# Kernel tuning notes

Hardware: AMD Instinct MI355X
Metric: run time of the kernel (lower is better)

The kernel has to match this reference:

```python
import jax, jax.numpy as jnp
import numpy as np

D, H, KVH, HD = 2048, 16, 8, 128
D1, D2 = 32, 64  # get_decompose_dim(2048)
BITS = 8


def fake_quant(x, bits=BITS):
    # per-row (last-axis) symmetric fake quant with straight-through estimator
    qmax = float(2 ** (bits - 1) - 1)
    s = jnp.maximum(jnp.max(jnp.abs(x), axis=-1, keepdims=True) / qmax, 1e-8)
    q = jnp.clip(jnp.round(x / s), -qmax, qmax) * s
    return x + jax.lax.stop_gradient(q - x)


def rotate_half(x):
    h = x.shape[-1] // 2
    return jnp.concatenate([-x[..., h:], x[..., :h]], axis=-1)


def setup_inputs() -> dict:
    key = jax.random.key(0)
    ks = jax.random.split(key, 10)
    B, S = 1, 2048
    hidden_states = jax.random.normal(ks[0], (B, S, D), jnp.float32)
    # rotary embeddings
    inv_freq = 1.0 / (10000.0 ** (jnp.arange(0, HD, 2, dtype=jnp.float32) / HD))
    t = jnp.arange(S, dtype=jnp.float32)
    freqs = t[:, None] * inv_freq[None, :]
    emb = jnp.concatenate([freqs, freqs], axis=-1)
    cos, sin = jnp.cos(emb)[None], jnp.sin(emb)[None]  # [1,S,HD]
    # projection weights
    Wq = jax.random.normal(ks[1], (H * HD, D), jnp.float32) * 0.02
    Wk = jax.random.normal(ks[2], (KVH * HD, D), jnp.float32) * 0.02
    Wv = jax.random.normal(ks[3], (KVH * HD, D), jnp.float32) * 0.02
    Wo = jax.random.normal(ks[4], (D, H * HD), jnp.float32) * 0.02
    # learned invertible transforms (near-identity for conditioning)
    L = jnp.eye(D1) + 0.02 * jax.random.normal(ks[5], (D1, D1), jnp.float32)
    R = jnp.eye(D2) + 0.02 * jax.random.normal(ks[6], (D2, D2), jnp.float32)
    diag = 1.0 + 0.1 * jax.random.uniform(ks[7], (D,), jnp.float32)
    Tk = jnp.eye(HD) + 0.02 * jax.random.normal(ks[8], (HD, HD), jnp.float32)
    Tv = jnp.eye(HD) + 0.02 * jax.random.normal(ks[9], (HD, HD), jnp.float32)
    return dict(hidden_states=hidden_states, cos=cos, sin=sin, Wq=Wq, Wk=Wk,
                Wv=Wv, Wo=Wo, L=L, R=R, diag=diag, Tk=Tk, Tv=Tv)


def reference(hidden_states, cos, sin, Wq, Wk, Wv, Wo, L, R, diag, Tk, Tv):
    B, S, _ = hidden_states.shape
    groups = H // KVH
    scale = HD ** -0.5
    # ---- ln_trans: x' = (x * diag) @ kron(L, R) ----
    P = diag[:, None] * jnp.kron(L, R)               # [D, D]
    Pinv = jnp.kron(jnp.linalg.inv(L), jnp.linalg.inv(R)) * (1.0 / diag)[None, :]
    x = hidden_states @ P
    x_q = fake_quant(x)                               # per-token activation quant
    # ---- QKV with transform fused into weights (qa_trans), then weight quant ----
    q = x_q @ fake_quant(Wq @ Pinv.T).T               # [B,S,H*HD]
    k = x_q @ fake_quant(Wk @ Pinv.T).T               # [B,S,KVH*HD]
    Wv_eff = jnp.einsum('hd,khD->kdD', Tv, (Wv @ Pinv.T).reshape(KVH, HD, D))
    v = x_q @ fake_quant(Wv_eff.reshape(KVH * HD, D)).T  # v already in Tv space
    # ---- heads + RoPE ----
    q = q.reshape(B, S, H, HD).transpose(0, 2, 1, 3)
    k = k.reshape(B, S, KVH, HD).transpose(0, 2, 1, 3)
    v = v.reshape(B, S, KVH, HD).transpose(0, 2, 1, 3)
    c, s_ = cos[:, None], sin[:, None]                # [1,1,S,HD]
    q = q * c + rotate_half(q) * s_
    k = k * c + rotate_half(k) * s_
    # ---- kcache trans + quant: q @ inv(Tk)^T, k @ Tk (dot product preserved) ----
    q = q @ jnp.linalg.inv(Tk).T
    k = fake_quant(k @ Tk)
    v = fake_quant(v)
    # ---- eager causal attention with GQA ----
    k = jnp.repeat(k, groups, axis=1)
    v = jnp.repeat(v, groups, axis=1)
    scores = jnp.einsum('bhqd,bhkd->bhqk', q, k) * scale
    mask = jnp.tril(jnp.ones((S, S), bool))
    scores = jnp.where(mask, scores, jnp.finfo(scores.dtype).min)
    w = jax.nn.softmax(scores, axis=-1)
    o = jnp.einsum('bhqk,bhkd->bhqd', w, v)
    o = o.transpose(0, 2, 1, 3).reshape(B, S, H * HD)
    # ---- undo vcache trans per head, then quantized o_proj ----
    o = (o.reshape(B, S, H, HD) @ jnp.linalg.inv(Tv)).reshape(B, S, H * HD)
    out = fake_quant(o) @ fake_quant(Wo).T
    return out
```

## Files before the change

### kernel.cpp

```cpp
#include <hip/hip_runtime.h>
#include <math.h>

typedef unsigned short u16;
typedef __attribute__((ext_vector_type(8))) short bf16x8;
typedef __attribute__((ext_vector_type(4))) float f32x4;

__device__ __forceinline__ u16 f2bf(float x) {
    union { float f; unsigned int u; } c; c.f = x;
    unsigned int r = c.u + 0x7fffu + ((c.u >> 16) & 1u);
    return (u16)(r >> 16);
}
__device__ __forceinline__ float bf2f(u16 h) {
    union { unsigned int u; float f; } c; c.u = ((unsigned int)h) << 16;
    return c.f;
}
__device__ __forceinline__ bf16x8 ld16(const u16* p) {
    bf16x8 r;
    ((uint2*)&r)[0] = *(const uint2*)p;
    ((uint2*)&r)[1] = *(const uint2*)(p + 4);
    return r;
}
__device__ __forceinline__ void st8(u16* dst, uint4 r) {
    *(uint2*)dst = make_uint2(r.x, r.y);
    *(uint2*)(dst + 4) = make_uint2(r.z, r.w);
}
__device__ __forceinline__ void cvt8(const float4& v0, const float4& v1,
                                     uint4& hi, uint4& lo) {
    float vv[8] = {v0.x, v0.y, v0.z, v0.w, v1.x, v1.y, v1.z, v1.w};
    u16 h[8], l[8];
#pragma unroll
    for (int e = 0; e < 8; ++e) {
        h[e] = f2bf(vv[e]);
        l[e] = f2bf(vv[e] - bf2f(h[e]));
    }
    hi.x = h[0] | ((unsigned)h[1] << 16); hi.y = h[2] | ((unsigned)h[3] << 16);
    hi.z = h[4] | ((unsigned)h[5] << 16); hi.w = h[6] | ((unsigned)h[7] << 16);
    lo.x = l[0] | ((unsigned)l[1] << 16); lo.y = l[2] | ((unsigned)l[3] << 16);
    lo.z = l[4] | ((unsigned)l[5] << 16); lo.w = l[6] | ((unsigned)l[7] << 16);
}

__global__ __launch_bounds__(1024) void p0_kernel(
    const float* __restrict__ A0, float* __restrict__ I0,
    const float* __restrict__ A1, float* __restrict__ I1,
    const float* __restrict__ A2, float* __restrict__ I2,
    const float* __restrict__ A3, float* __restrict__ I3,
    const float* __restrict__ X, const float* __restrict__ dg,
    const float* __restrict__ Lk, const float* __restrict__ Rk,
    u16* __restrict__ Yq, float* __restrict__ Ysc) {
    const int tid = threadIdx.x;
    if (blockIdx.x < 4) {
        __shared__ float rowbuf[2][128];
        const float* A; float* out; int N;
        switch (blockIdx.x) {
            case 0:  A = A0; out = I0; N = 32;  break;
            case 1:  A = A1; out = I1; N = 64;  break;
            case 2:  A = A2; out = I2; N = 128; break;
            default: A = A3; out = I3; N = 128; break;
        }
        const int i = tid >> 3, g = tid & 7, c0 = g * 16;
        const int rl = (i & 7) << 3;
        float r[16];
#pragma unroll
        for (int e = 0; e < 16; ++e) {
            int j = c0 + e;
            r[e] = (i < N && j < N) ? A[i * N + j] : ((i == j) ? 1.0f : 0.0f);
        }
        if (i == 0) {
            float ip = 1.0f / __shfl(r[0], rl, 64);
#pragma unroll
            for (int e = 0; e < 16; ++e)
                rowbuf[0][c0 + e] = (c0 + e == 0) ? ip : r[e] * ip;
        }
        __syncthreads();
        const int ng = N >> 4;
        for (int k16 = 0; k16 < ng; ++k16) {
#pragma unroll
            for (int e = 0; e < 16; ++e) {
                const int k = (k16 << 4) + e;
                const int pb = k & 1;
                float ci = __shfl(r[e], rl + k16, 64);
                float4 rb0 = *(const float4*)&rowbuf[pb][c0];
                float4 rb1 = *(const float4*)&rowbuf[pb][c0 + 4];
                float4 rb2 = *(const float4*)&rowbuf[pb][c0 + 8];
                float4 rb3 = *(const float4*)&rowbuf[pb][c0 + 12];
                float rb[16] = {rb0.x, rb0.y, rb0.z, rb0.w, rb1.x, rb1.y, rb1.z, rb1.w,
                                rb2.x, rb2.y, rb2.z, rb2.w, rb3.x, rb3.y, rb3.z, rb3.w};
                if (i == k) {
#pragma unroll
                    for (int e2 = 0; e2 < 16; ++e2) r[e2] = rb[e2];
                } else {
#pragma unroll
                    for (int e2 = 0; e2 < 16; ++e2) {
                        float v = (c0 + e2 == k) ? 0.0f : r[e2];
                        r[e2] = fmaf(-ci, rb[e2], v);
                    }
                }
                if (k + 1 < N && i == k + 1) {
                    const int en = (e + 1) & 15;
                    const int gn = (e == 15) ? k16 + 1 : k16;
                    float ip = 1.0f / __shfl(r[en], rl + gn, 64);
#pragma unroll
                    for (int e2 = 0; e2 < 16; ++e2)
                        rowbuf[pb ^ 1][c0 + e2] = (c0 + e2 == k + 1) ? ip : r[e2] * ip;
                }
                __syncthreads();
            }
        }
        if (i < N)
#pragma unroll
            for (int e = 0; e < 16; ++e) {
                int j = c0 + e;
                if (j < N) out[i * N + j] = r[e];
            }
    } else {
        __shared__ float Al[32 * 33];
        __shared__ float Bl[64 * 65];
        __shared__ float Xl[32 * 65];
        __shared__ float Tl[32 * 65];
        __shared__ float red[1024];
        if (tid < 1024) {
            int c = tid >> 5, a = tid & 31;
            Al[c * 33 + a] = Lk[c * 32 + a];
        }
        for (int idx = tid; idx < 4096; idx += 1024) {
            int d = idx >> 6, b = idx & 63;
            Bl[d * 65 + b] = Rk[d * 64 + b];
        }
        const int row = blockIdx.x - 4;
        const float* xp = X + (size_t)row * 2048;
        for (int j = tid; j < 2048; j += 1024)
            Xl[(j >> 6) * 65 + (j & 63)] = xp[j] * dg[j];
        __syncthreads();

        float t2[2], y2[2];
#pragma unroll
        for (int o = 0; o < 2; ++o) {
            int idx = tid * 2 + o;
            int c = idx >> 6, b = idx & 63;
            float acc = 0.0f;
            for (int d = 0; d < 64; ++d)
                acc = fmaf(Xl[c * 65 + d], Bl[d * 65 + b], acc);
            t2[o] = acc;
        }
        {
            int idx0 = tid * 2;
            Tl[(idx0 >> 6) * 65 + (idx0 & 63)] = t2[0];
            Tl[((idx0 + 1) >> 6) * 65 + ((idx0 + 1) & 63)] = t2[1];
        }
        __syncthreads();
#pragma unroll
        for (int o = 0; o < 2; ++o) {
            int idx = tid * 2 + o;
            int a = idx >> 6, b = idx & 63;
            float acc = 0.0f;
            for (int c2 = 0; c2 < 32; ++c2)
                acc = fmaf(Al[c2 * 33 + a], Tl[c2 * 65 + b], acc);
            y2[o] = acc;
        }
        float am = fmaxf(fabsf(y2[0]), fabsf(y2[1]));
        red[tid] = am;
        __syncthreads();
        for (int s = 512; s > 0; s >>= 1) {
            if (tid < s) red[tid] = fmaxf(red[tid], red[tid + s]);
            __syncthreads();
        }
        float scale = fmaxf(red[0] / 127.0f, 1e-8f);
        if (tid == 0) Ysc[row] = scale;
        unsigned pk;
        {
            float v0 = rintf(y2[0] / scale);
            v0 = fminf(fmaxf(v0, -127.0f), 127.0f);
            float v1 = rintf(y2[1] / scale);
            v1 = fminf(fmaxf(v1, -127.0f), 127.0f);
            pk = f2bf(v0) | ((unsigned)f2bf(v1) << 16);
        }
        *(unsigned*)(Yq + (size_t)row * 2048 + tid * 2) = pk;
    }
}

template <int TA, int TB, int OUTQ, int DIV>
__global__ __launch_bounds__(256) void kron_kernel(
    const float* __restrict__ X, const float* __restrict__ scIn,
    const float* __restrict__ A, const float* __restrict__ B,
    u16* __restrict__ Yq, float* __restrict__ Ysc, float* __restrict__ Yf) {
    __shared__ float Al[32 * 33];
    __shared__ float Bl[64 * 65];
    __shared__ float Xl[32 * 65];
    __shared__ float Tl[32 * 65];
    __shared__ float red[256];
    const int tid = threadIdx.x;
    for (int idx = tid; idx < 1024; idx += 256) {
        int c = idx >> 5, a = idx & 31;
        Al[c * 33 + a] = TA ? A[a * 32 + c] : A[c * 32 + a];
    }
    for (int idx = tid; idx < 4096; idx += 256) {
        int d = idx >> 6, b = idx & 63;
        Bl[d * 65 + b] = TB ? B[b * 64 + d] : B[d * 64 + b];
    }
    const int row = blockIdx.x;
    const float* xp = X + (size_t)row * 2048;
    for (int j = tid; j < 2048; j += 256) {
        float sc = DIV ? (1.0f / scIn[j]) : scIn[j];
        Xl[(j >> 6) * 65 + (j & 63)] = xp[j] * sc;
    }
    __syncthreads();

    const int c = tid >> 3, b0 = (tid & 7) * 8;
    float t[8];
#pragma unroll
    for (int jj = 0; jj < 8; ++jj) t[jj] = 0.0f;
    for (int d = 0; d < 64; ++d) {
        float xv = Xl[c * 65 + d];
#pragma unroll
        for (int jj = 0; jj < 8; ++jj)
            t[jj] = fmaf(xv, Bl[d * 65 + b0 + jj], t[jj]);
    }
#pragma unroll
    for (int jj = 0; jj < 8; ++jj) Tl[c * 65 + b0 + jj] = t[jj];
    __syncthreads();

    const int a = tid >> 3;
    float y[8];
#pragma unroll
    for (int jj = 0; jj < 8; ++jj) y[jj] = 0.0f;
    for (int c2 = 0; c2 < 32; ++c2) {
        float av = Al[c2 * 33 + a];
#pragma unroll
        for (int jj = 0; jj < 8; ++jj)
            y[jj] = fmaf(av, Tl[c2 * 65 + b0 + jj], y[jj]);
    }

    if (OUTQ) {
        float am = 0.0f;
#pragma unroll
        for (int jj = 0; jj < 8; ++jj) am = fmaxf(am, fabsf(y[jj]));
        red[tid] = am;
        __syncthreads();
        for (int s = 128; s > 0; s >>= 1) {
            if (tid < s) red[tid] = fmaxf(red[tid], red[tid + s]);
            __syncthreads();
        }
        float scale = fmaxf(red[0] / 127.0f, 1e-8f);
        if (tid == 0) Ysc[row] = scale;
        u16 qq[8];
#pragma unroll
        for (int e = 0; e < 8; ++e) {
            float v = rintf(y[e] / scale);
            v = fminf(fmaxf(v, -127.0f), 127.0f);
            qq[e] = f2bf(v);
        }
        uint4 pk;
        pk.x = qq[0] | ((unsigned)qq[1] << 16); pk.y = qq[2] | ((unsigned)qq[3] << 16);
        pk.z = qq[4] | ((unsigned)qq[5] << 16); pk.w = qq[6] | ((unsigned)qq[7] << 16);
        *(uint4*)(Yq + (size_t)row * 2048 + tid * 8) = pk;
    } else {
        float* yp = Yf + (size_t)row * 2048 + tid * 8;
        *(float4*)yp = make_float4(y[0], y[1], y[2], y[3]);
        *(float4*)(yp + 4) = make_float4(y[4], y[5], y[6], y[7]);
    }
}

__global__ void split_s_kernel(const float* __restrict__ in, int ld, int cols,
                               u16* __restrict__ hi, u16* __restrict__ lo) {
    int idx = (blockIdx.x * 256 + threadIdx.x) * 4;
    int r = idx / cols, c = idx % cols;
    float4 v = *(const float4*)(in + (size_t)r * ld + c);
    ushort4 h, l;
    h.x = f2bf(v.x); l.x = f2bf(v.x - bf2f(h.x));
    h.y = f2bf(v.y); l.y = f2bf(v.y - bf2f(h.y));
    h.z = f2bf(v.z); l.z = f2bf(v.z - bf2f(h.z));
    h.w = f2bf(v.w); l.w = f2bf(v.w - bf2f(h.w));
    *(ushort4*)(hi + idx) = h;
    *(ushort4*)(lo + idx) = l;
}

__global__ void split_t_kernel(const float* __restrict__ in, u16* __restrict__ hi,
                               u16* __restrict__ lo, int rows, int cols) {
    __shared__ float t[32][33];
    int bx = blockIdx.x, by = blockIdx.y;
    int lx = threadIdx.x & 31, ly = threadIdx.x >> 5;
    for (int r = ly; r < 32; r += 8)
        t[r][lx] = in[(size_t)(by * 32 + r) * cols + bx * 32 + lx];
    __syncthreads();
    for (int r = ly; r < 32; r += 8) {
        float v = t[lx][r];
        size_t o = (size_t)(bx * 32 + r) * rows + by * 32 + lx;
        u16 h = f2bf(v);
        hi[o] = h;
        lo[o] = f2bf(v - bf2f(h));
    }
}

__global__ void split_t3_kernel(const float* __restrict__ i0, u16* __restrict__ h0,
                                u16* __restrict__ l0,
                                const float* __restrict__ i1, u16* __restrict__ h1,
                                u16* __restrict__ l1,
                                const float* __restrict__ i2, u16* __restrict__ h2,
                                u16* __restrict__ l2) {
    __shared__ float t[32][33];
    const float* in; u16* hi; u16* lo;
    switch (blockIdx.z) {
        case 0:  in = i0; hi = h0; lo = l0; break;
        case 1:  in = i1; hi = h1; lo = l1; break;
        default: in = i2; hi = h2; lo = l2; break;
    }
    int bx = blockIdx.x, by = blockIdx.y;
    int lx = threadIdx.x & 31, ly = threadIdx.x >> 5;
    for (int r = ly; r < 32; r += 8)
        t[r][lx] = in[(size_t)(by * 32 + r) * 128 + bx * 32 + lx];
    __syncthreads();
    for (int r = ly; r < 32; r += 8) {
        float v = t[lx][r];
        size_t o = (size_t)(bx * 32 + r) * 128 + by * 32 + lx;
        u16 h = f2bf(v);
        hi[o] = h;
        lo[o] = f2bf(v - bf2f(h));
    }
}

__global__ __launch_bounds__(256) void gemm_kernel(
    const u16* __restrict__ Ah, const u16* __restrict__ Al, int lda, long aZ, int aDiv,
    const u16* __restrict__ Bh, const u16* __restrict__ Bl, int ldb, long bZ, int bDiv,
    float* __restrict__ C, int ldc, long cZ, int cDiv, int K, float alpha) {
    const int m0 = blockIdx.y * 128, n0 = blockIdx.x * 128;
    const int z = blockIdx.z;
    {
        long ao = (long)(z >> aDiv) * aZ;
        long bo = (long)(z >> bDiv) * bZ;
        Ah += ao; Al += ao; Bh += bo; Bl += bo;
    }
    __shared__ u16 Ash[2][2][128][36];
    __shared__ u16 Bsh[2][2][128][36];

    const int tid = threadIdx.x, lane = tid & 63, wave = tid >> 6;
    const int wr = wave >> 1, wc = wave & 1;
    const int fr = lane & 15, fg8 = (lane >> 4) * 8;
    const int srow = tid >> 2, cc8 = (tid & 3) * 8;

    f32x4 acc[4][4];
#pragma unroll
    for (int m = 0; m < 4; ++m)
#pragma unroll
        for (int n = 0; n < 4; ++n) acc[m][n] = (f32x4)0.0f;

    uint4 rah0, rah1, ral0, ral1, rbh0, rbh1, rbl0, rbl1;
    const size_t aoff0 = (size_t)(m0 + srow) * lda + cc8;
    const size_t aoff1 = aoff0 + (size_t)64 * lda;
    const size_t boff0 = (size_t)(n0 + srow) * ldb + cc8;
    const size_t boff1 = boff0 + (size_t)64 * ldb;

#define G_LOAD(k0) { \
    rah0 = *(const uint4*)(Ah + aoff0 + (k0)); rah1 = *(const uint4*)(Ah + aoff1 + (k0)); \
    ral0 = *(const uint4*)(Al + aoff0 + (k0)); ral1 = *(const uint4*)(Al + aoff1 + (k0)); \
    rbh0 = *(const uint4*)(Bh + boff0 + (k0)); rbh1 = *(const uint4*)(Bh + boff1 + (k0)); \
    rbl0 = *(const uint4*)(Bl + boff0 + (k0)); rbl1 = *(const uint4*)(Bl + boff1 + (k0)); }
#define G_STORE(b) { \
    st8(&Ash[b][0][srow][cc8], rah0); st8(&Ash[b][0][srow + 64][cc8], rah1); \
    st8(&Ash[b][1][srow][cc8], ral0); st8(&Ash[b][1][srow + 64][cc8], ral1); \
    st8(&Bsh[b][0][srow][cc8], rbh0); st8(&Bsh[b][0][srow + 64][cc8], rbh1); \
    st8(&Bsh[b][1][srow][cc8], rbl0); st8(&Bsh[b][1][srow + 64][cc8], rbl1); }

    const int nk = K >> 5;
    G_LOAD(0);
    G_STORE(0);
    __syncthreads();
    int cur = 0;
    for (int ik = 0; ik < nk; ++ik) {
        if (ik + 1 < nk) G_LOAD((ik + 1) << 5);
        bf16x8 bh[4], bl[4];
#pragma unroll
        for (int n = 0; n < 4; ++n) {
            bh[n] = ld16(&Bsh[cur][0][wc * 64 + n * 16 + fr][fg8]);
            bl[n] = ld16(&Bsh[cur][1][wc * 64 + n * 16 + fr][fg8]);
        }
#pragma unroll
        for (int m = 0; m < 4; ++m) {
            bf16x8 ah = ld16(&Ash[cur][0][wr * 64 + m * 16 + fr][fg8]);
            bf16x8 al = ld16(&Ash[cur][1][wr * 64 + m * 16 + fr][fg8]);
#pragma unroll
            for (int n = 0; n < 4; ++n) {
                acc[m][n] = __builtin_amdgcn_mfma_f32_16x16x32_bf16(ah, bh[n], acc[m][n], 0, 0, 0);
                acc[m][n] = __builtin_amdgcn_mfma_f32_16x16x32_bf16(ah, bl[n], acc[m][n], 0, 0, 0);
                acc[m][n] = __builtin_amdgcn_mfma_f32_16x16x32_bf16(al, bh[n], acc[m][n], 0, 0, 0);
            }
        }
        if (ik + 1 < nk) G_STORE(cur ^ 1);
        __syncthreads();
        cur ^= 1;
    }
    const long co = (long)(z >> cDiv) * cZ;
#pragma unroll
    for (int m = 0; m < 4; ++m) {
        int row_b = m0 + wr * 64 + m * 16 + (fg8 >> 1);
#pragma unroll
        for (int n = 0; n < 4; ++n) {
            int col = n0 + wc * 64 + n * 16 + fr;
#pragma unroll
            for (int j = 0; j < 4; ++j)
                C[co + (long)(row_b + j) * ldc + col] = alpha * acc[m][n][j];
        }
    }
#undef G_LOAD
#undef G_STORE
}

__global__ __launch_bounds__(256) void gemm_af32_kernel(
    const float* __restrict__ A, int lda, long aZ, int aDiv,
    const u16* __restrict__ Bh, const u16* __restrict__ Bl, int ldb, long bZ, int bDiv,
    float* __restrict__ C, int ldc, long cZ, int cDiv, int K, float alpha) {
    const int m0 = blockIdx.y * 128, n0 = blockIdx.x * 128;
    const int z = blockIdx.z;
    A += (long)(z >> aDiv) * aZ;
    {
        long bo = (long)(z >> bDiv) * bZ;
        Bh += bo; Bl += bo;
    }
    __shared__ u16 Ash[2][2][128][36];
    __shared__ u16 Bsh[2][2][128][36];

    const int tid = threadIdx.x, lane = tid & 63, wave = tid >> 6;
    const int wr = wave >> 1, wc = wave & 1;
    const int fr = lane & 15, fg8 = (lane >> 4) * 8;
    const int srow = tid >> 2, cc8 = (tid & 3) * 8;

    f32x4 acc[4][4];
#pragma unroll
    for (int m = 0; m < 4; ++m)
#pragma unroll
        for (int n = 0; n < 4; ++n) acc[m][n] = (f32x4)0.0f;

    float4 a00, a01, a10, a11;
    uint4 rbh0, rbh1, rbl0, rbl1;
    const size_t aoff0 = (size_t)(m0 + srow) * lda + cc8;
    const size_t aoff1 = aoff0 + (size_t)64 * lda;
    const size_t boff0 = (size_t)(n0 + srow) * ldb + cc8;
    const size_t boff1 = boff0 + (size_t)64 * ldb;

#define GA_LOAD(k0) { \
    a00 = *(const float4*)(A + aoff0 + (k0)); a01 = *(const float4*)(A + aoff0 + (k0) + 4); \
    a10 = *(const float4*)(A + aoff1 + (k0)); a11 = *(const float4*)(A + aoff1 + (k0) + 4); \
    rbh0 = *(const uint4*)(Bh + boff0 + (k0)); rbh1 = *(const uint4*)(Bh + boff1 + (k0)); \
    rbl0 = *(const uint4*)(Bl + boff0 + (k0)); rbl1 = *(const uint4*)(Bl + boff1 + (k0)); }
#define GA_STORE(b) { \
    uint4 h0_, l0_, h1_, l1_; \
    cvt8(a00, a01, h0_, l0_); cvt8(a10, a11, h1_, l1_); \
    st8(&Ash[b][0][srow][cc8], h0_); st8(&Ash[b][0][srow + 64][cc8], h1_); \
    st8(&Ash[b][1][srow][cc8], l0_); st8(&Ash[b][1][srow + 64][cc8], l1_); \
    st8(&Bsh[b][0][srow][cc8], rbh0); st8(&Bsh[b][0][srow + 64][cc8], rbh1); \
    st8(&Bsh[b][1][srow][cc8], rbl0); st8(&Bsh[b][1][srow + 64][cc8], rbl1); }

    const int nk = K >> 5;
    GA_LOAD(0);
    GA_STORE(0);
    __syncthreads();
    int cur = 0;
    for (int ik = 0; ik < nk; ++ik) {
        if (ik + 1 < nk) GA_LOAD((ik + 1) << 5);
        bf16x8 bh[4], bl[4];
#pragma unroll
        for (int n = 0; n < 4; ++n) {
            bh[n] = ld16(&Bsh[cur][0][wc * 64 + n * 16 + fr][fg8]);
            bl[n] = ld16(&Bsh[cur][1][wc * 64 + n * 16 + fr][fg8]);
        }
#pragma unroll
        for (int m = 0; m < 4; ++m) {
            bf16x8 ah = ld16(&Ash[cur][0][wr * 64 + m * 16 + fr][fg8]);
// ... 303 lines not shown
            int qg = qt * 64 + w * 16 + lc;
#pragma unroll
            for (int n = 0; n < 4; ++n)
#pragma unroll
                for (int j = 0; j < 4; ++j) {
                    int kgl = tg * 64 + n * 16 + lg * 4 + j;
                    if (kgl > qg) accs[n][j] = -3.0e38f;
                }
        }

        float pm = accs[0][0];
#pragma unroll
        for (int n = 0; n < 4; ++n)
#pragma unroll
            for (int j = 0; j < 4; ++j) pm = fmaxf(pm, accs[n][j]);
        pm = fmaxf(pm, __shfl_xor(pm, 16));
        pm = fmaxf(pm, __shfl_xor(pm, 32));
        bool need = pm > mj + THR;
        float mn = need ? pm : mj;
        float sf = need ? exp2f(mj - mn) : 1.0f;
        mj = mn;
        if (__any(need)) {
            float sfj[4];
#pragma unroll
            for (int j = 0; j < 4; ++j) sfj[j] = __shfl(sf, lg * 4 + j);
#pragma unroll
            for (int nn = 0; nn < 8; ++nn)
#pragma unroll
                for (int j = 0; j < 4; ++j) acc_o[nn][j] *= sfj[j];
        }
        float rowsum = 0.0f;
#pragma unroll
        for (int n = 0; n < 4; ++n)
#pragma unroll
            for (int j = 0; j < 4; ++j) {
                float p = exp2f(accs[n][j] - mj);
                accs[n][j] = p;
                rowsum += p;
            }
        rowsum += __shfl_xor(rowsum, 16);
        rowsum += __shfl_xor(rowsum, 32);
        lj = lj * sf + rowsum;

#pragma unroll
        for (int n = 0; n < 4; ++n)
#pragma unroll
            for (int jp = 0; jp < 2; ++jp) {
                int k = n * 16 + lg * 4 + jp * 2;
                unsigned val = f2bf(accs[n][jp * 2] * Vss[cur][k]) |
                               ((unsigned)f2bf(accs[n][jp * 2 + 1] * Vss[cur][k + 1]) << 16);
                int cch = k >> 3;
                *(unsigned*)(&Psh[w][lc * 64 + ((cch ^ (lc & 7)) << 3) + (k & 7)]) = val;
            }
        bf16x8 pf[2];
#pragma unroll
        for (int kk = 0; kk < 2; ++kk)
            pf[kk] = ld16(&Psh[w][lc * 64 + (((kk * 4 + lg) ^ (lc & 7)) << 3)]);

#pragma unroll
        for (int nn = 0; nn < 8; ++nn) {
            int d = nn * 16 + lc;
#pragma unroll
            for (int kk = 0; kk < 2; ++kk) {
                bf16x8 vf = ld16(&Vsh[cur][d * 64 + (((kk * 4 + lg) ^ (d & 7)) << 3)]);
                acc_o[nn] = __builtin_amdgcn_mfma_f32_16x16x32_bf16(pf[kk], vf, acc_o[nn], 0, 0, 0);
            }
        }
        if (t + 1 < tn) STAGE_WRITE(cur ^ 1);
        __syncthreads();
    }
#undef STAGE_LOAD
#undef STAGE_WRITE

    float* op = obuf + (size_t)part * 4194304 + ((size_t)h * 2048 + qt * 64 + w * 16) * 128;
#pragma unroll
    for (int nn = 0; nn < 8; ++nn)
#pragma unroll
        for (int j = 0; j < 4; ++j)
            op[(lg * 4 + j) * 128 + nn * 16 + lc] = acc_o[nn][j];
    if (lg == 0) {
        int rs = h * 2048 + qt * 64 + w * 16 + lc;
        mlbuf[part * 65536 + rs] = mj;
        mlbuf[part * 65536 + 32768 + rs] = lj;
    }
}

__global__ void combine_kernel(const float* __restrict__ o01,
                               const float* __restrict__ ml,
                               float* __restrict__ of) {
    int idx = blockIdx.x * 256 + threadIdx.x;
    int hs = idx >> 7;
    float m0 = ml[hs], l0 = ml[32768 + hs];
    float m1 = ml[65536 + hs], l1 = ml[98304 + hs];
    float m = fmaxf(m0, m1);
    float w0 = exp2f(m0 - m), w1 = exp2f(m1 - m);
    float l = l0 * w0 + l1 * w1;
    of[idx] = (o01[idx] * w0 + o01[4194304 + idx] * w1) / l;
}

__global__ void add2_kernel(const float* __restrict__ a, const float* __restrict__ b,
                            float* __restrict__ o) {
    int i = (blockIdx.x * 256 + threadIdx.x) * 4;
    float4 x = *(const float4*)(a + i);
    float4 y = *(const float4*)(b + i);
    x.x += y.x; x.y += y.y; x.z += y.z; x.w += y.w;
    *(float4*)(o + i) = x;
}

extern "C" void kernel_launch(void* const* d_in, const int* in_sizes, int n_in,
                              void* d_out, int out_size, void* d_ws, size_t ws_size,
                              hipStream_t stream) {
    const float* hidden = (const float*)d_in[0];
    const float* cosp   = (const float*)d_in[1];
    const float* sinp   = (const float*)d_in[2];
    const float* Wq     = (const float*)d_in[3];
    const float* Wk     = (const float*)d_in[4];
    const float* Wv     = (const float*)d_in[5];
    const float* Wo     = (const float*)d_in[6];
    const float* Lp     = (const float*)d_in[7];
    const float* Rp     = (const float*)d_in[8];
    const float* diag   = (const float*)d_in[9];
    const float* Tkp    = (const float*)d_in[10];
    const float* Tvp    = (const float*)d_in[11];
    float* out = (float*)d_out;

    const size_t MiB = 1ull << 20;
    char* W = (char*)d_ws;
    auto F = [&](size_t mb) { return (float*)(W + mb * MiB); };
    auto U = [&](size_t mb) { return (u16*)(W + mb * MiB); };
    const long HP2 = 2097152;

    float* dsc   = (float*)d_out;
    float* invL  = dsc;
    float* invR  = dsc + 1024;
    float* invTk = dsc + 5120;
    float* invTv = dsc + 21504;
    u16* sm = (u16*)(dsc + 37888);
    u16* invTk_sh = sm;              u16* invTk_sl = sm + 16384;
    u16* TkT_sh   = sm + 2 * 16384;  u16* TkT_sl   = sm + 3 * 16384;
    u16* invTvT_sh= sm + 4 * 16384;  u16* invTvT_sl= sm + 5 * 16384;
    u16* TvT_sh   = sm + 6 * 16384;  u16* TvT_sl   = sm + 7 * 16384;

    float* xs    = F(88);
    float* wqkvs = xs + 2048;
    float* wqs   = wqkvs;
    float* wks   = wqkvs + 2048;
    float* wvs   = wqkvs + 3072;
    float* k2s   = wqkvs + 4096;
    float* vs    = k2s + 16384;
    float* o2s   = vs + 16384;
    float* wos   = o2s + 2048;

    u16* Xi = U(0);
    p0_kernel<<<2052, 1024, 0, stream>>>(Lp, invL, Rp, invR, Tkp, invTk, Tvp, invTv,
                                         hidden, diag, Lp, Rp, Xi, xs);
    split_s_kernel<<<16, 256, 0, stream>>>(invTk, 128, 128, invTk_sh, invTk_sl);
    split_t3_kernel<<<dim3(4, 4, 3), 256, 0, stream>>>(
        Tkp, TkT_sh, TkT_sl, invTv, invTvT_sh, invTvT_sl, Tvp, TvT_sh, TvT_sl);

    u16* WQKVi = U(8);
    u16* WVi   = U(20);
    float* WvP = F(24);
    kron_kernel<1, 1, 1, 1><<<2048, 256, 0, stream>>>(Wq, diag, invL, invR, WQKVi, wqs, 0);
    kron_kernel<1, 1, 1, 1><<<1024, 256, 0, stream>>>(Wk, diag, invL, invR, U(16), wks, 0);
    kron_kernel<1, 1, 0, 1><<<1024, 256, 0, stream>>>(Wv, diag, invL, invR, 0, 0, WvP);

    u16* WVPt_s = U(32);
    split_t_kernel<<<dim3(64, 32), 256, 0, stream>>>(WvP, WVPt_s, WVPt_s + HP2, 1024, 2048);
    float* WVf = F(72);
    gemm_kernel<<<dim3(16, 1, 8), 256, 0, stream>>>(
        TvT_sh, TvT_sl, 128, 0, 0, WVPt_s, WVPt_s + HP2, 1024, 128, 0,
        WVf, 2048, (long)128 * 2048, 0, 128, 1.0f);
    rowquant_int_kernel<<<1024, 256, 0, stream>>>(WVf, WVi, wvs, 2048);

    float* QKVf = F(40);
    gemm_int_kernel<<<dim3(32, 16), 256, 0, stream>>>(Xi, 2048, xs, WQKVi, 2048, wqkvs,
                                                      QKVf, 4096, 0, 0, 0, 2048);

    rope_kernel<<<8192, 256, 0, stream>>>(QKVf, 4096, 0, cosp, sinp, 16);
    rope_kernel<<<4096, 256, 0, stream>>>(QKVf, 4096, 2048, cosp, sinp, 8);

    float* k2f = F(32);
    gemm_af32_kernel<<<dim3(1, 16, 8), 256, 0, stream>>>(
        QKVf + 2048, 4096, 128, 0, TkT_sh, TkT_sl, 128, 0, 0,
        k2f, 1024, 128, 0, 128, 1.0f);
    u16* k2i = U(8);
    rowquant_w_kernel<<<4096, 256, 0, stream>>>(k2f, k2i, k2s);

    u16* vTi = U(16);
    quantT_v_kernel<<<dim3(32, 8), 256, 0, stream>>>(QKVf, vTi, vs);

    float* q2f = F(72);
    gemm_af32_kernel<<<dim3(1, 16, 16), 256, 0, stream>>>(
        QKVf, 4096, 128, 0, invTk_sh, invTk_sl, 128, 0, 0,
        q2f, 2048, 128, 0, 128, 1.0f);

    float* o01 = F(40);
    float* ml  = F(32);
    flash_kernel<<<dim3(16, 2, 32), 256, 0, stream>>>(q2f, k2i, k2s, vTi, vs, o01, ml);
    float* of = F(0);
    combine_kernel<<<16384, 256, 0, stream>>>(o01, ml, of);

    float* o2f = F(16);
    gemm_af32_kernel<<<dim3(1, 16, 16), 256, 0, stream>>>(
        of, 128, 262144, 0, invTvT_sh, invTvT_sl, 128, 0, 0,
        o2f, 2048, 128, 0, 128, 1.0f);
    u16* o2i = U(32);
    rowquant_int_kernel<<<2048, 256, 0, stream>>>(o2f, o2i, o2s, 2048);
    u16* Woi = U(40);
    rowquant_int_kernel<<<2048, 256, 0, stream>>>(Wo, Woi, wos, 2048);
    float* C0 = F(48);
    gemm_int_kernel<<<dim3(16, 16, 2), 256, 0, stream>>>(o2i, 2048, o2s, Woi, 2048, wos,
                                                         C0, 2048, 1024, 1024, 4194304, 1024);
    add2_kernel<<<4096, 256, 0, stream>>>(C0, C0 + 4194304, out);

    (void)in_sizes; (void)n_in; (void)out_size; (void)ws_size;
}
```

Measured before the change: 459.5 us.

## Reschedule prologue kernels to overlap Tk/Tv inversion with weight kron transforms

```diff
diff --git a/kernel.cpp b/kernel.cpp
--- a/kernel.cpp
+++ b/kernel.cpp
@@ -39,124 +39,111 @@
     lo.z = l[4] | ((unsigned)l[5] << 16); lo.w = l[6] | ((unsigned)l[7] << 16);
 }
 
-__global__ __launch_bounds__(1024) void p0_kernel(
-    const float* __restrict__ A0, float* __restrict__ I0,
-    const float* __restrict__ A1, float* __restrict__ I1,
-    const float* __restrict__ A2, float* __restrict__ I2,
-    const float* __restrict__ A3, float* __restrict__ I3,
-    const float* __restrict__ X, const float* __restrict__ dg,
-    const float* __restrict__ Lk, const float* __restrict__ Rk,
-    u16* __restrict__ Yq, float* __restrict__ Ysc) {
-    const int tid = threadIdx.x;
-    if (blockIdx.x < 4) {
-        __shared__ float rowbuf[2][128];
-        const float* A; float* out; int N;
-        switch (blockIdx.x) {
-            case 0:  A = A0; out = I0; N = 32;  break;
-            case 1:  A = A1; out = I1; N = 64;  break;
-            case 2:  A = A2; out = I2; N = 128; break;
-            default: A = A3; out = I3; N = 128; break;
-        }
-        const int i = tid >> 3, g = tid & 7, c0 = g * 16;
-        const int rl = (i & 7) << 3;
-        float r[16];
+__device__ void gj_body(const float* __restrict__ A, float* __restrict__ out,
+                        int N, float (*rowbuf)[128], int tid) {
+    const int i = tid >> 3, g = tid & 7, c0 = g * 16;
+    const int rl = (i & 7) << 3;
+    float r[16];
+#pragma unroll
+    for (int e = 0; e < 16; ++e) {
+        int j = c0 + e;
+        r[e] = (i < N && j < N) ? A[i * N + j] : ((i == j) ? 1.0f : 0.0f);
+    }
+    if (i == 0) {
+        float ip = 1.0f / __shfl(r[0], rl, 64);
+#pragma unroll
+        for (int e = 0; e < 16; ++e)
+            rowbuf[0][c0 + e] = (c0 + e == 0) ? ip : r[e] * ip;
+    }
+    __syncthreads();
+    const int ng = N >> 4;
+    for (int k16 = 0; k16 < ng; ++k16) {
+#pragma unroll
+        for (int e = 0; e < 16; ++e) {
+            const int k = (k16 << 4) + e;
+            const int pb = k & 1;
+            float ci = __shfl(r[e], rl + k16, 64);
+            float4 rb0 = *(const float4*)&rowbuf[pb][c0];
+            float4 rb1 = *(const float4*)&rowbuf[pb][c0 + 4];
+            float4 rb2 = *(const float4*)&rowbuf[pb][c0 + 8];
+            float4 rb3 = *(const float4*)&rowbuf[pb][c0 + 12];
+            float rb[16] = {rb0.x, rb0.y, rb0.z, rb0.w, rb1.x, rb1.y, rb1.z, rb1.w,
+                            rb2.x, rb2.y, rb2.z, rb2.w, rb3.x, rb3.y, rb3.z, rb3.w};
+            if (i == k) {
+#pragma unroll
+                for (int e2 = 0; e2 < 16; ++e2) r[e2] = rb[e2];
+            } else {
+#pragma unroll
+                for (int e2 = 0; e2 < 16; ++e2) {
+                    float v = (c0 + e2 == k) ? 0.0f : r[e2];
+                    r[e2] = fmaf(-ci, rb[e2], v);
+                }
+            }
+            if (k + 1 < N && i == k + 1) {
+                const int en = (e + 1) & 15;
+                const int gn = (e == 15) ? k16 + 1 : k16;
+                float ip = 1.0f / __shfl(r[en], rl + gn, 64);
+#pragma unroll
+                for (int e2 = 0; e2 < 16; ++e2)
+                    rowbuf[pb ^ 1][c0 + e2] = (c0 + e2 == k + 1) ? ip : r[e2] * ip;
+            }
+            __syncthreads();
+        }
+    }
+    if (i < N)
 #pragma unroll
         for (int e = 0; e < 16; ++e) {
             int j = c0 + e;
-            r[e] = (i < N && j < N) ? A[i * N + j] : ((i == j) ? 1.0f : 0.0f);
-        }
-        if (i == 0) {
-            float ip = 1.0f / __shfl(r[0], rl, 64);
-#pragma unroll
-            for (int e = 0; e < 16; ++e)
-                rowbuf[0][c0 + e] = (c0 + e == 0) ? ip : r[e] * ip;
-        }
-        __syncthreads();
-        const int ng = N >> 4;
-        for (int k16 = 0; k16 < ng; ++k16) {
-#pragma unroll
-            for (int e = 0; e < 16; ++e) {
-                const int k = (k16 << 4) + e;
-                const int pb = k & 1;
-                float ci = __shfl(r[e], rl + k16, 64);
-                float4 rb0 = *(const float4*)&rowbuf[pb][c0];
-                float4 rb1 = *(const float4*)&rowbuf[pb][c0 + 4];
-                float4 rb2 = *(const float4*)&rowbuf[pb][c0 + 8];
-                float4 rb3 = *(const float4*)&rowbuf[pb][c0 + 12];
-                float rb[16] = {rb0.x, rb0.y, rb0.z, rb0.w, rb1.x, rb1.y, rb1.z, rb1.w,
-                                rb2.x, rb2.y, rb2.z, rb2.w, rb3.x, rb3.y, rb3.z, rb3.w};
-                if (i == k) {
-#pragma unroll
-                    for (int e2 = 0; e2 < 16; ++e2) r[e2] = rb[e2];
-                } else {
-#pragma unroll
-                    for (int e2 = 0; e2 < 16; ++e2) {
-                        float v = (c0 + e2 == k) ? 0.0f : r[e2];
-                        r[e2] = fmaf(-ci, rb[e2], v);
-                    }
-                }
-                if (k + 1 < N && i == k + 1) {
-                    const int en = (e + 1) & 15;
-                    const int gn = (e == 15) ? k16 + 1 : k16;
-                    float ip = 1.0f / __shfl(r[en], rl + gn, 64);
-#pragma unroll
-                    for (int e2 = 0; e2 < 16; ++e2)
-                        rowbuf[pb ^ 1][c0 + e2] = (c0 + e2 == k + 1) ? ip : r[e2] * ip;
-                }
-                __syncthreads();
-            }
-        }
-        if (i < N)
-#pragma unroll
-            for (int e = 0; e < 16; ++e) {
-                int j = c0 + e;
-                if (j < N) out[i * N + j] = r[e];
-            }
-    } else {
-        __shared__ float Al[32 * 33];
-        __shared__ float Bl[64 * 65];
-        __shared__ float Xl[32 * 65];
-        __shared__ float Tl[32 * 65];
-        __shared__ float red[1024];
-        if (tid < 1024) {
-            int c = tid >> 5, a = tid & 31;
-            Al[c * 33 + a] = Lk[c * 32 + a];
-        }
-        for (int idx = tid; idx < 4096; idx += 1024) {
-            int d = idx >> 6, b = idx & 63;
-            Bl[d * 65 + b] = Rk[d * 64 + b];
-        }
-        const int row = blockIdx.x - 4;
-        const float* xp = X + (size_t)row * 2048;
-        for (int j = tid; j < 2048; j += 1024)
-            Xl[(j >> 6) * 65 + (j & 63)] = xp[j] * dg[j];
-        __syncthreads();
-
-        float t2[2], y2[2];
-#pragma unroll
-        for (int o = 0; o < 2; ++o) {
-            int idx = tid * 2 + o;
-            int c = idx >> 6, b = idx & 63;
-            float acc = 0.0f;
-            for (int d = 0; d < 64; ++d)
-                acc = fmaf(Xl[c * 65 + d], Bl[d * 65 + b], acc);
-            t2[o] = acc;
-        }
-        {
-            int idx0 = tid * 2;
-            Tl[(idx0 >> 6) * 65 + (idx0 & 63)] = t2[0];
-            Tl[((idx0 + 1) >> 6) * 65 + ((idx0 + 1) & 63)] = t2[1];
-        }
-        __syncthreads();
-#pragma unroll
-        for (int o = 0; o < 2; ++o) {
-            int idx = tid * 2 + o;
-            int a = idx >> 6, b = idx & 63;
-            float acc = 0.0f;
-            for (int c2 = 0; c2 < 32; ++c2)
-                acc = fmaf(Al[c2 * 33 + a], Tl[c2 * 65 + b], acc);
-            y2[o] = acc;
-        }
+            if (j < N) out[i * N + j] = r[e];
+        }
+}
+
+template <int TA, int TB, int OUTQ, int DIV>
+__device__ void kron1024_body(const float* __restrict__ X, const float* __restrict__ scIn,
+                              const float* __restrict__ A, const float* __restrict__ B,
+                              u16* __restrict__ Yq, float* __restrict__ Ysc,
+                              float* __restrict__ Yf, int row, int tid,
+                              float* Al, float* Bl, float* Xl, float* Tl, float* red) {
+    {
+        int c = tid >> 5, a = tid & 31;
+        Al[c * 33 + a] = TA ? A[a * 32 + c] : A[c * 32 + a];
+    }
+    for (int idx = tid; idx < 4096; idx += 1024) {
+        int d = idx >> 6, b = idx & 63;
+        Bl[d * 65 + b] = TB ? B[b * 64 + d] : B[d * 64 + b];
+    }
+    const float* xp = X + (size_t)row * 2048;
+    for (int j = tid; j < 2048; j += 1024) {
+        float sc = DIV ? (1.0f / scIn[j]) : scIn[j];
+        Xl[(j >> 6) * 65 + (j & 63)] = xp[j] * sc;
+    }
+    __syncthreads();
+    float t2[2], y2[2];
+#pragma unroll
+    for (int o = 0; o < 2; ++o) {
+        int idx = tid * 2 + o;
+        int c = idx >> 6, b = idx & 63;
+        float acc = 0.0f;
+        for (int d = 0; d < 64; ++d)
+            acc = fmaf(Xl[c * 65 + d], Bl[d * 65 + b], acc);
+        t2[o] = acc;
+    }
+    {
+        int idx0 = tid * 2;
+        Tl[(idx0 >> 6) * 65 + (idx0 & 63)] = t2[0];
+        Tl[((idx0 + 1) >> 6) * 65 + ((idx0 + 1) & 63)] = t2[1];
+    }
+    __syncthreads();
+#pragma unroll
+    for (int o = 0; o < 2; ++o) {
+        int idx = tid * 2 + o;
+        int a = idx >> 6, b = idx & 63;
+        float acc = 0.0f;
+        for (int c2 = 0; c2 < 32; ++c2)
+            acc = fmaf(Al[c2 * 33 + a], Tl[c2 * 65 + b], acc);
+        y2[o] = acc;
+    }
+    if (OUTQ) {
         float am = fmaxf(fabsf(y2[0]), fabsf(y2[1]));
         red[tid] = am;
         __syncthreads();
@@ -166,112 +153,107 @@
         }
         float scale = fmaxf(red[0] / 127.0f, 1e-8f);
         if (tid == 0) Ysc[row] = scale;
-        unsigned pk;
-        {
-            float v0 = rintf(y2[0] / scale);
-            v0 = fminf(fmaxf(v0, -127.0f), 127.0f);
-            float v1 = rintf(y2[1] / scale);
-            v1 = fminf(fmaxf(v1, -127.0f), 127.0f);
-            pk = f2bf(v0) | ((unsigned)f2bf(v1) << 16);
-        }
+        float v0 = rintf(y2[0] / scale);
+        v0 = fminf(fmaxf(v0, -127.0f), 127.0f);
+        float v1 = rintf(y2[1] / scale);
+        v1 = fminf(fmaxf(v1, -127.0f), 127.0f);
+        unsigned pk = f2bf(v0) | ((unsigned)f2bf(v1) << 16);
         *(unsigned*)(Yq + (size_t)row * 2048 + tid * 2) = pk;
-    }
-}
-
-template <int TA, int TB, int OUTQ, int DIV>
-__global__ __launch_bounds__(256) void kron_kernel(
-    const float* __restrict__ X, const float* __restrict__ scIn,
-    const float* __restrict__ A, const float* __restrict__ B,
-    u16* __restrict__ Yq, float* __restrict__ Ysc, float* __restrict__ Yf) {
+    } else {
+        Yf[(size_t)row * 2048 + tid * 2] = y2[0];
+        Yf[(size_t)row * 2048 + tid * 2 + 1] = y2[1];
+    }
+}
+
+__global__ __launch_bounds__(1024) void p0a_kernel(
+    const float* __restrict__ Lp, float* __restrict__ invL,
+    const float* __restrict__ Rp, float* __restrict__ invR,
+    const float* __restrict__ hidden, const float* __restrict__ dg,
+    u16* __restrict__ Xi, float* __restrict__ xs,
+    const float* __restrict__ Tkp, u16* __restrict__ TkT_sh, u16* __restrict__ TkT_sl,
+    const float* __restrict__ Tvp, u16* __restrict__ TvT_sh, u16* __restrict__ TvT_sl) {
+    __shared__ float rowbuf[2][128];
     __shared__ float Al[32 * 33];
     __shared__ float Bl[64 * 65];
     __shared__ float Xl[32 * 65];
     __shared__ float Tl[32 * 65];
-    __shared__ float red[256];
+    __shared__ float red[1024];
     const int tid = threadIdx.x;
-    for (int idx = tid; idx < 1024; idx += 256) {
-        int c = idx >> 5, a = idx & 31;
-        Al[c * 33 + a] = TA ? A[a * 32 + c] : A[c * 32 + a];
-    }
-    for (int idx = tid; idx < 4096; idx += 256) {
-        int d = idx >> 6, b = idx & 63;
-        Bl[d * 65 + b] = TB ? B[b * 64 + d] : B[d * 64 + b];
-    }
-    const int row = blockIdx.x;
-    const float* xp = X + (size_t)row * 2048;
-    for (int j = tid; j < 2048; j += 256) {
-        float sc = DIV ? (1.0f / scIn[j]) : scIn[j];
-        Xl[(j >> 6) * 65 + (j & 63)] = xp[j] * sc;
-    }
-    __syncthreads();
-
-    const int c = tid >> 3, b0 = (tid & 7) * 8;
-    float t[8];
-#pragma unroll
-    for (int jj = 0; jj < 8; ++jj) t[jj] = 0.0f;
-    for (int d = 0; d < 64; ++d) {
-        float xv = Xl[c * 65 + d];
-#pragma unroll
-        for (int jj = 0; jj < 8; ++jj)
-            t[jj] = fmaf(xv, Bl[d * 65 + b0 + jj], t[jj]);
-    }
-#pragma unroll
-    for (int jj = 0; jj < 8; ++jj) Tl[c * 65 + b0 + jj] = t[jj];
-    __syncthreads();
-
-    const int a = tid >> 3;
-    float y[8];
-#pragma unroll
-    for (int jj = 0; jj < 8; ++jj) y[jj] = 0.0f;
-    for (int c2 = 0; c2 < 32; ++c2) {
-        float av = Al[c2 * 33 + a];
-#pragma unroll
-        for (int jj = 0; jj < 8; ++jj)
-            y[jj] = fmaf(av, Tl[c2 * 65 + b0 + jj], y[jj]);
-    }
-
-    if (OUTQ) {
-        float am = 0.0f;
-#pragma unroll
-        for (int jj = 0; jj < 8; ++jj) am = fmaxf(am, fabsf(y[jj]));
-        red[tid] = am;
-        __syncthreads();
-        for (int s = 128; s > 0; s >>= 1) {
-            if (tid < s) red[tid] = fmaxf(red[tid], red[tid + s]);
-            __syncthreads();
-        }
-        float scale = fmaxf(red[0] / 127.0f, 1e-8f);
-        if (tid == 0) Ysc[row] = scale;
-        u16 qq[8];
-#pragma unroll
-        for (int e = 0; e < 8; ++e) {
-            float v = rintf(y[e] / scale);
-            v = fminf(fmaxf(v, -127.0f), 127.0f);
-            qq[e] = f2bf(v);
-        }
-        uint4 pk;
-        pk.x = qq[0] | ((unsigned)qq[1] << 16); pk.y = qq[2] | ((unsigned)qq[3] << 16);
-        pk.z = qq[4] | ((unsigned)qq[5] << 16); pk.w = qq[6] | ((unsigned)qq[7] << 16);
-        *(uint4*)(Yq + (size_t)row * 2048 + tid * 8) = pk;
+    const int b = blockIdx.x;
+    if (b == 0) {
+        gj_body(Lp, invL, 32, rowbuf, tid);
+    } else if (b == 1) {
+        gj_body(Rp, invR, 64, rowbuf, tid);
+    } else if (b < 2050) {
+        kron1024_body<0, 0, 1, 0>(hidden, dg, Lp, Rp, Xi, xs, 0, b - 2, tid,
+                                  Al, Bl, Xl, Tl, red);
     } else {
-        float* yp = Yf + (size_t)row * 2048 + tid * 8;
-        *(float4*)yp = make_float4(y[0], y[1], y[2], y[3]);
-        *(float4*)(yp + 4) = make_float4(y[4], y[5], y[6], y[7]);
-    }
-}
-
-__global__ void split_s_kernel(const float* __restrict__ in, int ld, int cols,
-                               u16* __restrict__ hi, u16* __restrict__ lo) {
-    int idx = (blockIdx.x * 256 + threadIdx.x) * 4;
-    int r = idx / cols, c = idx % cols;
-    float4 v = *(const float4*)(in + (size_t)r * ld + c);
-    ushort4 h, l;
-    h.x = f2bf(v.x); l.x = f2bf(v.x - bf2f(h.x));
-    h.y = f2bf(v.y); l.y = f2bf(v.y - bf2f(h.y));
-    h.z = f2bf(v.z); l.z = f2bf(v.z - bf2f(h.z));
-    h.w = f2bf(v.w); l.w = f2bf(v.w - bf2f(h.w));
-    *(ushort4*)(hi + idx) = h;
-    *(ushort4*)(lo + idx) = l;
+        const float* in = (b == 2050) ? Tkp : Tvp;
+        u16* hi = (b == 2050) ? TkT_sh : TvT_sh;
+        u16* lo = (b == 2050) ? TkT_sl : TvT_sl;
+        for (int idx = tid; idx < 16384; idx += 1024) {
+            int r = idx >> 7, c = idx & 127;
+            float v = in[r * 128 + c];
+            u16 h = f2bf(v);
+            hi[c * 128 + r] = h;
+            lo[c * 128 + r] = f2bf(v - bf2f(h));
+        }
+    }
+}
+
+__global__ __launch_bounds__(1024) void p0b_kernel(
+    const float* __restrict__ Tkp, float* __restrict__ invTk,
+    const float* __restrict__ Tvp, float* __restrict__ invTv,
+    const float* __restrict__ Wq, const float* __restrict__ Wk,
+    const float* __restrict__ Wv, const float* __restrict__ dg,
+    const float* __restrict__ invL, const float* __restrict__ invR,
+    u16* __restrict__ WQi, float* __restrict__ wqs,
+    u16* __restrict__ WKi, float* __restrict__ wks,
+    float* __restrict__ WvP) {
+    __shared__ float rowbuf[2][128];
+    __shared__ float Al[32 * 33];
+    __shared__ float Bl[64 * 65];
+    __shared__ float Xl[32 * 65];
+    __shared__ float Tl[32 * 65];
+    __shared__ float red[1024];
+    const int tid = threadIdx.x;
+    const int b = blockIdx.x;
+    if (b == 0) {
+        gj_body(Tkp, invTk, 128, rowbuf, tid);
+    } else if (b == 1) {
+        gj_body(Tvp, invTv, 128, rowbuf, tid);
+    } else if (b < 2050) {
+        kron1024_body<1, 1, 1, 1>(Wq, dg, invL, invR, WQi, wqs, 0, b - 2, tid,
+                                  Al, Bl, Xl, Tl, red);
+    } else if (b < 3074) {
+        kron1024_body<1, 1, 1, 1>(Wk, dg, invL, invR, WKi, wks, 0, b - 2050, tid,
+                                  Al, Bl, Xl, Tl, red);
+    } else {
+        kron1024_body<1, 1, 0, 1>(Wv, dg, invL, invR, 0, 0, WvP, b - 3074, tid,
+                                  Al, Bl, Xl, Tl, red);
+    }
+}
+
+__global__ __launch_bounds__(1024) void ps_kernel(
+    const float* __restrict__ invTk, u16* __restrict__ ik_h, u16* __restrict__ ik_l,
+    const float* __restrict__ invTv, u16* __restrict__ ivT_h, u16* __restrict__ ivT_l) {
+    const int tid = threadIdx.x;
+    if (blockIdx.x == 0) {
+        for (int idx = tid; idx < 16384; idx += 1024) {
+            float v = invTk[idx];
+            u16 h = f2bf(v);
+            ik_h[idx] = h;
+            ik_l[idx] = f2bf(v - bf2f(h));
+        }
+    } else {
+        for (int idx = tid; idx < 16384; idx += 1024) {
+            int r = idx >> 7, c = idx & 127;
+            float v = invTv[r * 128 + c];
+            u16 h = f2bf(v);
+            ivT_h[c * 128 + r] = h;
+            ivT_l[c * 128 + r] = f2bf(v - bf2f(h));
+        }
+    }
 }
 
 __global__ void split_t_kernel(const float* __restrict__ in, u16* __restrict__ hi,
@@ -285,33 +267,6 @@
     for (int r = ly; r < 32; r += 8) {
         float v = t[lx][r];
         size_t o = (size_t)(bx * 32 + r) * rows + by * 32 + lx;
-        u16 h = f2bf(v);
-        hi[o] = h;
-        lo[o] = f2bf(v - bf2f(h));
-    }
-}
-
-__global__ void split_t3_kernel(const float* __restrict__ i0, u16* __restrict__ h0,
-                                u16* __restrict__ l0,
-                                const float* __restrict__ i1, u16* __restrict__ h1,
-                                u16* __restrict__ l1,
-                                const float* __restrict__ i2, u16* __restrict__ h2,
-                                u16* __restrict__ l2) {
-    __shared__ float t[32][33];
-    const float* in; u16* hi; u16* lo;
-    switch (blockIdx.z) {
-        case 0:  in = i0; hi = h0; lo = l0; break;
-        case 1:  in = i1; hi = h1; lo = l1; break;
-        default: in = i2; hi = h2; lo = l2; break;
-    }
-    int bx = blockIdx.x, by = blockIdx.y;
-    int lx = threadIdx.x & 31, ly = threadIdx.x >> 5;
-    for (int r = ly; r < 32; r += 8)
-        t[r][lx] = in[(size_t)(by * 32 + r) * 128 + bx * 32 + lx];
-    __syncthreads();
-    for (int r = ly; r < 32; r += 8) {
-        float v = t[lx][r];
-        size_t o = (size_t)(bx * 32 + r) * 128 + by * 32 + lx;
         u16 h = f2bf(v);
         hi[o] = h;
         lo[o] = f2bf(v - bf2f(h));
@@ -921,18 +876,17 @@
     float* wos   = o2s + 2048;
 
     u16* Xi = U(0);
-    p0_kernel<<<2052, 1024, 0, stream>>>(Lp, invL, Rp, invR, Tkp, invTk, Tvp, invTv,
-                                         hidden, diag, Lp, Rp, Xi, xs);
-    split_s_kernel<<<16, 256, 0, stream>>>(invTk, 128, 128, invTk_sh, invTk_sl);
-    split_t3_kernel<<<dim3(4, 4, 3), 256, 0, stream>>>(
-        Tkp, TkT_sh, TkT_sl, invTv, invTvT_sh, invTvT_sl, Tvp, TvT_sh, TvT_sl);
+    p0a_kernel<<<2052, 1024, 0, stream>>>(Lp, invL, Rp, invR, hidden, diag, Xi, xs,
+                                          Tkp, TkT_sh, TkT_sl, Tvp, TvT_sh, TvT_sl);
 
     u16* WQKVi = U(8);
     u16* WVi   = U(20);
     float* WvP = F(24);
-    kron_kernel<1, 1, 1, 1><<<2048, 256, 0, stream>>>(Wq, diag, invL, invR, WQKVi, wqs, 0);
-    kron_kernel<1, 1, 1, 1><<<1024, 256, 0, stream>>>(Wk, diag, invL, invR, U(16), wks, 0);
-    kron_kernel<1, 1, 0, 1><<<1024, 256, 0, stream>>>(Wv, diag, invL, invR, 0, 0, WvP);
+    p0b_kernel<<<4098, 1024, 0, stream>>>(Tkp, invTk, Tvp, invTv, Wq, Wk, Wv, diag,
+                                          invL, invR, WQKVi, wqs, U(16), wks, WvP);
+
+    ps_kernel<<<2, 1024, 0, stream>>>(invTk, invTk_sh, invTk_sl,
+                                      invTv, invTvT_sh, invTvT_sl);
 
     u16* WVPt_s = U(32);
     split_t_kernel<<<dim3(64, 32), 256, 0, stream>>>(WvP, WVPt_s, WVPt_s + HP2, 1024, 2048);
```

Result: slower. 531.5 us (+15.7%).
